# Kernel tuning notes

Measured on AMD Instinct MI355X. Metric: run time of the kernel, lower is better.

Reference implementation:

```python
import jax, jax.numpy as jnp
import numpy as np

B, T, I, H, HORIZON = 64, 512, 256, 1024, 24


def _lstm_layer(x, Wih, Whh, bih, bhh):
    """PyTorch-convention LSTM layer. x: [B,T,I_l] -> outputs [B,T,H].
    Gate order along 4H axis: i, f, g, o."""
    b = x.shape[0]
    h_dim = Whh.shape[1]
    # Precompute input contribution for all timesteps: [B,T,4H]
    xg = jnp.einsum('bti,gi->btg', x, Wih) + bih + bhh

    def step(carry, xg_t):
        h, c = carry
        gates = xg_t + h @ Whh.T  # [B,4H]
        i_g, f_g, g_g, o_g = jnp.split(gates, 4, axis=-1)
        c = jax.nn.sigmoid(f_g) * c + jax.nn.sigmoid(i_g) * jnp.tanh(g_g)
        h = jax.nn.sigmoid(o_g) * jnp.tanh(c)
        return (h, c), h

    h0 = jnp.zeros((b, h_dim), x.dtype)
    (_, _), hs = jax.lax.scan(step, (h0, h0), jnp.swapaxes(xg, 0, 1))
    return jnp.swapaxes(hs, 0, 1)  # [B,T,H]


def setup_inputs() -> dict:
    key = jax.random.key(0)
    ks = jax.random.split(key, 11)
    s_i = 1.0 / np.sqrt(H)  # PyTorch-style uniform-ish scale, use scaled normal
    return {
        'x': jax.random.normal(ks[0], (B, T, I), jnp.float32),
        'W_ih0': jax.random.normal(ks[1], (4 * H, I), jnp.float32) * s_i,
        'W_hh0': jax.random.normal(ks[2], (4 * H, H), jnp.float32) * s_i,
        'b_ih0': jax.random.normal(ks[3], (4 * H,), jnp.float32) * s_i,
        'b_hh0': jax.random.normal(ks[4], (4 * H,), jnp.float32) * s_i,
        'W_ih1': jax.random.normal(ks[5], (4 * H, H), jnp.float32) * s_i,
        'W_hh1': jax.random.normal(ks[6], (4 * H, H), jnp.float32) * s_i,
        'b_ih1': jax.random.normal(ks[7], (4 * H,), jnp.float32) * s_i,
        'b_hh1': jax.random.normal(ks[8], (4 * H,), jnp.float32) * s_i,
        'W_head': jax.random.normal(ks[9], (HORIZON, H), jnp.float32) * s_i,
        'b_head': jax.random.normal(ks[10], (HORIZON,), jnp.float32) * s_i,
    }


def reference(x, W_ih0, W_hh0, b_ih0, b_hh0, W_ih1, W_hh1, b_ih1, b_hh1, W_head, b_head):
    h1 = _lstm_layer(x, W_ih0, W_hh0, b_ih0, b_hh0)   # [B,T,H]
    h2 = _lstm_layer(h1, W_ih1, W_hh1, b_ih1, b_hh1)  # [B,T,H]
    last = h2[:, -1, :]                                # [B,H]
    return last @ W_head.T + b_head                    # [B,HORIZON]
```

## Files before the change

### kernel.cpp

```cpp
#include <hip/hip_runtime.h>


typedef _Float16 h8 __attribute__((ext_vector_type(8)));
typedef float    f4 __attribute__((ext_vector_type(4)));
typedef unsigned long long u64;

#define WS_W0P   0
#define WS_W1P   10485760
#define WS_H0Q   27262976
#define WS_H2Q   27787264
#define WS_SYNC  28049408
#define WS_XPK   28057600
#define WS_XPK_END 44834816ULL

static __device__ __forceinline__ float sigm(float v) { return 1.f / (1.f + __expf(-v)); }
static __device__ __forceinline__ float tanh_fast(float v) {
  const float e = __expf(2.f * v);
  return 1.f - 2.f / (e + 1.f);
}
static __device__ __forceinline__ h8 vload16(const _Float16* p) {
  return *(const volatile h8*)p;
}
static __device__ __forceinline__ void vstore16(_Float16* p, h8 v) {
  *(volatile h8*)p = v;
}

__global__ void prep_kernel(const float* __restrict__ x,
                            const float* __restrict__ Wih0, const float* __restrict__ Whh0,
                            const float* __restrict__ Wih1, const float* __restrict__ Whh1,
                            _Float16* __restrict__ W0p, _Float16* __restrict__ W1p,
                            _Float16* __restrict__ xpk,
                            unsigned* __restrict__ hz, unsigned* __restrict__ sync_ws)
{
  const long tid0 = (long)blockIdx.x * blockDim.x + threadIdx.x;
  const long np   = (long)gridDim.x * blockDim.x;

  for (long e = tid0; e < 5242880; e += np) {
    const int j = e & 7, quad = (e >> 3) & 3, l15 = (e >> 5) & 15, nt = (e >> 9) & 7;
    const int r = (int)(e >> 12);
    const int c = r % 40, cs = r / 40;
    const int col = nt * 16 + l15;
    const int row = (col >> 5) * 1024 + cs * 32 + (col & 31);
    const int k = c * 32 + quad * 8 + j;
    const float v = (k < 256) ? Wih0[(long)row * 256 + k] : Whh0[(long)row * 1024 + k - 256];
    W0p[e] = (_Float16)v;
  }
  for (long e = tid0; e < 8388608; e += np) {
    const int j = e & 7, quad = (e >> 3) & 3, l15 = (e >> 5) & 15, nt = (e >> 9) & 7;
    const int r = (int)(e >> 12);
    const int c = r & 63, cs = r >> 6;
    const int col = nt * 16 + l15;
    const int row = (col >> 5) * 1024 + cs * 32 + (col & 31);
    const int k = c * 32 + quad * 8 + j;
    const float v = (k < 1024) ? Wih1[(long)row * 1024 + k] : Whh1[(long)row * 1024 + k - 1024];
    W1p[e] = (_Float16)v;
  }
  if (xpk) {
    for (long e = tid0; e < 8388608; e += np) {
      const int k32 = e & 31, b16 = (e >> 5) & 15, bg = (e >> 9) & 3;
      const int c = (e >> 11) & 7;
      const int t = (int)(e >> 14);
      const int b = bg * 16 + b16, k = c * 32 + k32;
      xpk[e] = (_Float16)x[(long)b * 131072 + (long)t * 256 + k];
    }
  }
  for (long e = tid0; e < 196608; e += np) hz[e] = 0u;
  if (tid0 < 2048) sync_ws[tid0] = 0u;
}

template<bool XP>
__launch_bounds__(512, 1)
__global__ void lstm_kernel(const float* __restrict__ x, const _Float16* __restrict__ xpk,
                            const float* __restrict__ bih0, const float* __restrict__ bhh0,
                            const float* __restrict__ bih1, const float* __restrict__ bhh1,
                            const _Float16* __restrict__ W0p, const _Float16* __restrict__ W1p,
                            _Float16* __restrict__ h0q, _Float16* __restrict__ h2q,
                            unsigned* __restrict__ sy)
{
  extern __shared__ float gb[];
  __shared__ float cst[512];
  __shared__ float biasl[128];
  __shared__ _Float16 htmp[32 * 18];

  const int tid = threadIdx.x, wg = blockIdx.x;
  const int xcd = wg & 7, jdec = wg >> 3;
  const int lay = jdec & 1, jj = jdec >> 1;
  const int bg = jj & 3, csl = jj >> 2;
  const int cs = xcd * 4 + csl;
  const int lane = tid & 63, kg = tid >> 6;
  const int l15 = lane & 15, quad = lane >> 4;
  const int boff = l15 * 32 + quad * 8;
  const int aoff = bg * 512 + l15 * 32 + quad * 8;

  const _Float16* Wp = lay ? (W1p + (long)cs * 262144) : (W0p + (long)cs * 163840);

  if (tid < 128) {
    const int row = (tid >> 5) * 1024 + cs * 32 + (tid & 31);
    biasl[tid] = lay ? (bih1[row] + bhh1[row]) : (bih0[row] + bhh0[row]);
  }
  cst[tid] = 0.f;
  __syncthreads();

  unsigned* const fL0  = sy + (bg * 32);
  unsigned* const fL1  = sy + ((4 + bg) * 32);
  unsigned* const fOwn = (lay ? fL1 : fL0) + cs;

  auto spin1 = [&](const unsigned* p, int tgt) {
    while ((int)__hip_atomic_load(p, __ATOMIC_RELAXED, __HIP_MEMORY_SCOPE_AGENT) < tgt)
      __builtin_amdgcn_s_sleep(2);
  };

  auto dump = [&](const f4* acc) {
#pragma unroll
    for (int nt = 0; nt < 8; ++nt)
      *(f4*)&gb[(kg * 128 + nt * 16 + l15) * 24 + quad * 4] = acc[nt];
  };

  auto pointwise_publish = [&](_Float16* wr, int n, int gtgt) {
    __syncthreads();
    {
      const int b16 = tid & 15, hh = tid >> 4;
      float gv[4];
#pragma unroll
      for (int gt = 0; gt < 4; ++gt) {
        float s = biasl[gt * 32 + hh];
#pragma unroll
        for (int k = 0; k < 8; ++k) s += gb[(k * 128 + gt * 32 + hh) * 24 + b16];
        gv[gt] = s;
      }
      const float si = sigm(gv[0]), sf = sigm(gv[1]);
      const float tg = tanh_fast(gv[2]), so = sigm(gv[3]);
      const float cn = sf * cst[tid] + si * tg;
      cst[tid] = cn;
      htmp[hh * 18 + b16] = (_Float16)(so * tanh_fast(cn));
    }
    __syncthreads();
    if (tid < 64) {
      if (tid < 32) spin1(fL1 + tid, gtgt);
      const int b16 = tid & 15, q = tid >> 4;
      union { h8 v; _Float16 e[8]; } r;
#pragma unroll
      for (int i = 0; i < 8; ++i) r.e[i] = htmp[(q * 8 + i) * 18 + b16];
      vstore16(wr + (cs * 4 + bg) * 512 + b16 * 32 + q * 8, r.v);
      asm volatile("s_waitcnt vmcnt(0)" ::: "memory");
      if (tid == 0)
        __hip_atomic_store(fOwn, (unsigned)(n + 1),
                           __ATOMIC_RELAXED, __HIP_MEMORY_SCOPE_AGENT);
    }
  };

  if (lay == 0) {
    const int c0 = kg * 5;
    for (int n = 0; n < 512; ++n) {
      const _Float16* h0prev = h0q + ((n - 1) & 3) * 65536;
      const _Float16* xs = XP ? (xpk + (long)n * 16384) : nullptr;

      f4 acc[8] = {};
      h8 Ab[5]; h8 Bb[2][8];
      auto loadB = [&](int c, int sl) {
        const _Float16* bp = Wp + (long)c * 4096 + boff;
#pragma unroll
        for (int nt = 0; nt < 8; ++nt) Bb[sl][nt] = *(const h8*)(bp + nt * 512);
      };
      auto loadA = [&](int c, int idx) {
        if (c < 8) {
          if (XP) Ab[idx] = *(const h8*)(xs + c * 2048 + aoff);
          else {
            const float* q = x + (long)(bg * 16 + l15) * 131072 + (long)n * 256 + c * 32 + quad * 8;
            const f4 v0 = *(const f4*)q;
            const f4 v1 = *(const f4*)(q + 4);
            h8 t;
            t[0]=(_Float16)v0[0]; t[1]=(_Float16)v0[1]; t[2]=(_Float16)v0[2]; t[3]=(_Float16)v0[3];
            t[4]=(_Float16)v1[0]; t[5]=(_Float16)v1[1]; t[6]=(_Float16)v1[2]; t[7]=(_Float16)v1[3];
            Ab[idx] = t;
          }
        } else {
          Ab[idx] = vload16(h0prev + (c - 8) * 2048 + aoff);
        }
      };

      loadB(c0, 0);
#pragma unroll
      for (int i = 0; i < 5; ++i)
        if (c0 + i < 8) loadA(c0 + i, i);

      if (lane < 5) {
        const int c = c0 + lane;
        if (c >= 8) spin1(fL0 + (c - 8), n);
      }

#pragma unroll
      for (int i = 0; i < 5; ++i)
        if (c0 + i >= 8) loadA(c0 + i, i);

#pragma unroll
      for (int i = 0; i < 5; ++i) {
        if (i + 1 < 5) loadB(c0 + i + 1, (i + 1) & 1);
        const h8 A = Ab[i];
#pragma unroll
        for (int nt = 0; nt < 8; ++nt)
          acc[nt] = __builtin_amdgcn_mfma_f32_16x16x32_f16(A, Bb[i & 1][nt], acc[nt], 0, 0, 0);
      }
      dump(acc);
      pointwise_publish(h0q + (n & 3) * 65536, n, n - 3);
    }
  } else {
    const int c0 = kg * 4;
    for (int n = 0; n < 512; ++n) {
      const _Float16* h0cur  = h0q + (n & 3) * 65536;
      const _Float16* h2prev = h2q + ((n - 1) & 1) * 65536;

      f4 acc[8] = {};
      h8 Ab[4]; h8 Bb[2][8];
      auto loadB = [&](int c, int sl) {
        const _Float16* bp = Wp + (long)c * 4096 + boff;
#pragma unroll
        for (int nt = 0; nt < 8; ++nt) Bb[sl][nt] = *(const h8*)(bp + nt * 512);
      };
      auto loadA = [&](const _Float16* hb, int cloc, int idx) {
        Ab[idx] = vload16(hb + cloc * 2048 + aoff);
      };

      loadB(c0, 0);
      if (lane < 4) spin1(fL0 + c0 + lane, n + 1);
#pragma unroll
      for (int i = 0; i < 4; ++i) loadA(h0cur, c0 + i, i);
#pragma unroll
      for (int i = 0; i < 4; ++i) {
        if (i + 1 < 4) loadB(c0 + i + 1, (i + 1) & 1);
        const h8 A = Ab[i];
#pragma unroll
        for (int nt = 0; nt < 8; ++nt)
          acc[nt] = __builtin_amdgcn_mfma_f32_16x16x32_f16(A, Bb[i & 1][nt], acc[nt], 0, 0, 0);
      }

      loadB(32 + c0, 0);
      if (lane < 4) spin1(fL1 + c0 + lane, n);
#pragma unroll
      for (int i = 0; i < 4; ++i) loadA(h2prev, c0 + i, i);
#pragma unroll
      for (int i = 0; i < 4; ++i) {
        if (i + 1 < 4) loadB(32 + c0 + i + 1, (i + 1) & 1);
        const h8 A = Ab[i];
#pragma unroll
        for (int nt = 0; nt < 8; ++nt)
          acc[nt] = __builtin_amdgcn_mfma_f32_16x16x32_f16(A, Bb[i & 1][nt], acc[nt], 0, 0, 0);
      }
      dump(acc);
      pointwise_publish(h2q + (n & 1) * 65536, n, n);
    }
  }
}

__global__ void head_kernel(const _Float16* __restrict__ h2s, const float* __restrict__ Wh,
                            const float* __restrict__ bh, float* __restrict__ out)
{
  const int blk = blockIdx.x;
  const int b = blk / 24, j = blk % 24;
  const int lane = threadIdx.x;
  float sum = 0.f;
#pragma unroll
  for (int k0 = 0; k0 < 1024; k0 += 64) {
    const int hid = k0 + lane;
    const float hv = (float)h2s[((hid >> 5) * 4 + (b >> 4)) * 512 + (b & 15) * 32 + (hid & 31)];
    sum += hv * Wh[(long)j * 1024 + hid];
  }
#pragma unroll
  for (int off = 32; off > 0; off >>= 1)
    sum += __shfl_down(sum, off, 64);
  if (lane == 0) out[b * 24 + j] = sum + bh[j];
}

extern "C" void kernel_launch(void* const* d_in, const int* in_sizes, int n_in,
                              void* d_out, int out_size, void* d_ws, size_t ws_size,
                              hipStream_t stream)
{
  const float* x    = (const float*)d_in[0];
  const float* Wih0 = (const float*)d_in[1];
  const float* Whh0 = (const float*)d_in[2];
  const float* bih0 = (const float*)d_in[3];
  const float* bhh0 = (const float*)d_in[4];
  const float* Wih1 = (const float*)d_in[5];
  const float* Whh1 = (const float*)d_in[6];
  const float* bih1 = (const float*)d_in[7];
  const float* bhh1 = (const float*)d_in[8];
  const float* Whd  = (const float*)d_in[9];
  const float* bhd  = (const float*)d_in[10];

  char* ws = (char*)d_ws;
  _Float16* W0p     = (_Float16*)(ws + WS_W0P);
  _Float16* W1p     = (_Float16*)(ws + WS_W1P);
  _Float16* h0q     = (_Float16*)(ws + WS_H0Q);
  _Float16* h2q     = (_Float16*)(ws + WS_H2Q);
  unsigned* sync_ws = (unsigned*)(ws + WS_SYNC);
  float* out = (float*)d_out;

  const bool use_xpk = (ws_size >= WS_XPK_END);
  _Float16* xpk = use_xpk ? (_Float16*)(ws + WS_XPK) : nullptr;

  prep_kernel<<<dim3(2048), dim3(256), 0, stream>>>(
      x, Wih0, Whh0, Wih1, Whh1, W0p, W1p, xpk,
      (unsigned*)(ws + WS_H0Q), sync_ws);

  if (use_xpk)
    lstm_kernel<true><<<dim3(256), dim3(512), 98304, stream>>>(
        x, xpk, bih0, bhh0, bih1, bhh1, W0p, W1p, h0q, h2q, sync_ws);
  else
    lstm_kernel<false><<<dim3(256), dim3(512), 98304, stream>>>(
        x, nullptr, bih0, bhh0, bih1, bhh1, W0p, W1p, h0q, h2q, sync_ws);

  head_kernel<<<dim3(64 * 24), dim3(64), 0, stream>>>(
      h2q + 65536, Whd, bhd, out);
}
```

Measured before the change: 4.564 ms.

## Free one warp per block from MFMA work and prefetch all B tiles upfront

```diff
diff --git a/kernel.cpp b/kernel.cpp
--- a/kernel.cpp
+++ b/kernel.cpp
@@ -107,13 +107,13 @@
 
   auto spin1 = [&](const unsigned* p, int tgt) {
     while ((int)__hip_atomic_load(p, __ATOMIC_RELAXED, __HIP_MEMORY_SCOPE_AGENT) < tgt)
-      __builtin_amdgcn_s_sleep(2);
+      __builtin_amdgcn_s_sleep(1);
   };
 
   auto dump = [&](const f4* acc) {
 #pragma unroll
     for (int nt = 0; nt < 8; ++nt)
-      *(f4*)&gb[(kg * 128 + nt * 16 + l15) * 24 + quad * 4] = acc[nt];
+      *(f4*)&gb[((kg - 1) * 128 + nt * 16 + l15) * 24 + quad * 4] = acc[nt];
   };
 
   auto pointwise_publish = [&](_Float16* wr, int n, int gtgt) {
@@ -125,7 +125,7 @@
       for (int gt = 0; gt < 4; ++gt) {
         float s = biasl[gt * 32 + hh];
 #pragma unroll
-        for (int k = 0; k < 8; ++k) s += gb[(k * 128 + gt * 32 + hh) * 24 + b16];
+        for (int k = 0; k < 7; ++k) s += gb[(k * 128 + gt * 32 + hh) * 24 + b16];
         gv[gt] = s;
       }
       const float si = sigm(gv[0]), sf = sigm(gv[1]);
@@ -150,103 +150,107 @@
   };
 
   if (lay == 0) {
-    const int c0 = kg * 5;
+    const int c0 = (kg <= 6) ? (kg - 1) * 6 : 35;
+    const int nc = (kg <= 5) ? 6 : 5;
     for (int n = 0; n < 512; ++n) {
-      const _Float16* h0prev = h0q + ((n - 1) & 3) * 65536;
-      const _Float16* xs = XP ? (xpk + (long)n * 16384) : nullptr;
-
-      f4 acc[8] = {};
-      h8 Ab[5]; h8 Bb[2][8];
-      auto loadB = [&](int c, int sl) {
-        const _Float16* bp = Wp + (long)c * 4096 + boff;
-#pragma unroll
-        for (int nt = 0; nt < 8; ++nt) Bb[sl][nt] = *(const h8*)(bp + nt * 512);
-      };
-      auto loadA = [&](int c, int idx) {
-        if (c < 8) {
-          if (XP) Ab[idx] = *(const h8*)(xs + c * 2048 + aoff);
-          else {
-            const float* q = x + (long)(bg * 16 + l15) * 131072 + (long)n * 256 + c * 32 + quad * 8;
-            const f4 v0 = *(const f4*)q;
-            const f4 v1 = *(const f4*)(q + 4);
-            h8 t;
-            t[0]=(_Float16)v0[0]; t[1]=(_Float16)v0[1]; t[2]=(_Float16)v0[2]; t[3]=(_Float16)v0[3];
-            t[4]=(_Float16)v1[0]; t[5]=(_Float16)v1[1]; t[6]=(_Float16)v1[2]; t[7]=(_Float16)v1[3];
-            Ab[idx] = t;
+      if (kg >= 1) {
+        const _Float16* h0prev = h0q + ((n - 1) & 3) * 65536;
+        const _Float16* xs = XP ? (xpk + (long)n * 16384) : nullptr;
+
+        f4 acc[8] = {};
+        h8 Ab[6]; h8 Bb[6][8];
+        auto loadB = [&](int c, int sl) {
+          const _Float16* bp = Wp + (long)c * 4096 + boff;
+#pragma unroll
+          for (int nt = 0; nt < 8; ++nt) Bb[sl][nt] = *(const h8*)(bp + nt * 512);
+        };
+        auto loadA = [&](int c, int idx) {
+          if (c < 8) {
+            if (XP) Ab[idx] = *(const h8*)(xs + c * 2048 + aoff);
+            else {
+              const float* q = x + (long)(bg * 16 + l15) * 131072 + (long)n * 256 + c * 32 + quad * 8;
+              const f4 v0 = *(const f4*)q;
+              const f4 v1 = *(const f4*)(q + 4);
+              h8 t;
+              t[0]=(_Float16)v0[0]; t[1]=(_Float16)v0[1]; t[2]=(_Float16)v0[2]; t[3]=(_Float16)v0[3];
+              t[4]=(_Float16)v1[0]; t[5]=(_Float16)v1[1]; t[6]=(_Float16)v1[2]; t[7]=(_Float16)v1[3];
+              Ab[idx] = t;
+            }
+          } else {
+            Ab[idx] = vload16(h0prev + (c - 8) * 2048 + aoff);
           }
-        } else {
-          Ab[idx] = vload16(h0prev + (c - 8) * 2048 + aoff);
+        };
+
+#pragma unroll
+        for (int i = 0; i < 6; ++i) if (i < nc) loadB(c0 + i, i);
+#pragma unroll
+        for (int i = 0; i < 6; ++i) if (i < nc && (c0 + i) < 8) loadA(c0 + i, i);
+
+        if (lane < nc) {
+          const int c = c0 + lane;
+          if (c >= 8) spin1(fL0 + (c - 8), n);
         }
-      };
-
-      loadB(c0, 0);
-#pragma unroll
-      for (int i = 0; i < 5; ++i)
-        if (c0 + i < 8) loadA(c0 + i, i);
-
-      if (lane < 5) {
-        const int c = c0 + lane;
-        if (c >= 8) spin1(fL0 + (c - 8), n);
+
+#pragma unroll
+        for (int i = 0; i < 6; ++i) if (i < nc && (c0 + i) >= 8) loadA(c0 + i, i);
+
+#pragma unroll
+        for (int i = 0; i < 6; ++i) if (i < nc) {
+          const h8 A = Ab[i];
+#pragma unroll
+          for (int nt = 0; nt < 8; ++nt)
+            acc[nt] = __builtin_amdgcn_mfma_f32_16x16x32_f16(A, Bb[i][nt], acc[nt], 0, 0, 0);
+        }
+        dump(acc);
       }
-
-#pragma unroll
-      for (int i = 0; i < 5; ++i)
-        if (c0 + i >= 8) loadA(c0 + i, i);
-
-#pragma unroll
-      for (int i = 0; i < 5; ++i) {
-        if (i + 1 < 5) loadB(c0 + i + 1, (i + 1) & 1);
-        const h8 A = Ab[i];
-#pragma unroll
-        for (int nt = 0; nt < 8; ++nt)
-          acc[nt] = __builtin_amdgcn_mfma_f32_16x16x32_f16(A, Bb[i & 1][nt], acc[nt], 0, 0, 0);
+      pointwise_publish(h0q + (n & 3) * 65536, n, n - 3);
+    }
+  } else {
+    const int c0 = (kg <= 5) ? (kg - 1) * 5 : 20 + (kg - 5) * 4;
+    const int nc = (kg <= 4) ? 5 : 4;
+    for (int n = 0; n < 512; ++n) {
+      if (kg >= 1) {
+        const _Float16* h0cur  = h0q + (n & 3) * 65536;
+        const _Float16* h2prev = h2q + ((n - 1) & 1) * 65536;
+
+        f4 acc[8] = {};
+        h8 Ab[5]; h8 Bb[5][8];
+        auto loadB = [&](int c, int sl) {
+          const _Float16* bp = Wp + (long)c * 4096 + boff;
+#pragma unroll
+          for (int nt = 0; nt < 8; ++nt) Bb[sl][nt] = *(const h8*)(bp + nt * 512);
+        };
+        auto loadA = [&](const _Float16* hb, int cloc, int idx) {
+          Ab[idx] = vload16(hb + cloc * 2048 + aoff);
+        };
+
+#pragma unroll
+        for (int i = 0; i < 5; ++i) if (i < nc) loadB(c0 + i, i);
+        if (lane < nc) spin1(fL0 + c0 + lane, n + 1);
+#pragma unroll
+        for (int i = 0; i < 5; ++i) if (i < nc) loadA(h0cur, c0 + i, i);
+#pragma unroll
+        for (int i = 0; i < 5; ++i) if (i < nc) {
+          const h8 A = Ab[i];
+#pragma unroll
+          for (int nt = 0; nt < 8; ++nt)
+            acc[nt] = __builtin_amdgcn_mfma_f32_16x16x32_f16(A, Bb[i][nt], acc[nt], 0, 0, 0);
+        }
+
+#pragma unroll
+        for (int i = 0; i < 5; ++i) if (i < nc) loadB(32 + c0 + i, i);
+        if (lane < nc) spin1(fL1 + c0 + lane, n);
+#pragma unroll
+        for (int i = 0; i < 5; ++i) if (i < nc) loadA(h2prev, c0 + i, i);
+#pragma unroll
+        for (int i = 0; i < 5; ++i) if (i < nc) {
+          const h8 A = Ab[i];
+#pragma unroll
+          for (int nt = 0; nt < 8; ++nt)
+            acc[nt] = __builtin_amdgcn_mfma_f32_16x16x32_f16(A, Bb[i][nt], acc[nt], 0, 0, 0);
+        }
+        dump(acc);
       }
-      dump(acc);
-      pointwise_publish(h0q + (n & 3) * 65536, n, n - 3);
-    }
-  } else {
-    const int c0 = kg * 4;
-    for (int n = 0; n < 512; ++n) {
-      const _Float16* h0cur  = h0q + (n & 3) * 65536;
-      const _Float16* h2prev = h2q + ((n - 1) & 1) * 65536;
-
-      f4 acc[8] = {};
-      h8 Ab[4]; h8 Bb[2][8];
-      auto loadB = [&](int c, int sl) {
-        const _Float16* bp = Wp + (long)c * 4096 + boff;
-#pragma unroll
-        for (int nt = 0; nt < 8; ++nt) Bb[sl][nt] = *(const h8*)(bp + nt * 512);
-      };
-      auto loadA = [&](const _Float16* hb, int cloc, int idx) {
-        Ab[idx] = vload16(hb + cloc * 2048 + aoff);
-      };
-
-      loadB(c0, 0);
-      if (lane < 4) spin1(fL0 + c0 + lane, n + 1);
-#pragma unroll
-      for (int i = 0; i < 4; ++i) loadA(h0cur, c0 + i, i);
-#pragma unroll
-      for (int i = 0; i < 4; ++i) {
-        if (i + 1 < 4) loadB(c0 + i + 1, (i + 1) & 1);
-        const h8 A = Ab[i];
-#pragma unroll
-        for (int nt = 0; nt < 8; ++nt)
-          acc[nt] = __builtin_amdgcn_mfma_f32_16x16x32_f16(A, Bb[i & 1][nt], acc[nt], 0, 0, 0);
-      }
-
-      loadB(32 + c0, 0);
-      if (lane < 4) spin1(fL1 + c0 + lane, n);
-#pragma unroll
-      for (int i = 0; i < 4; ++i) loadA(h2prev, c0 + i, i);
-#pragma unroll
-      for (int i = 0; i < 4; ++i) {
-        if (i + 1 < 4) loadB(32 + c0 + i + 1, (i + 1) & 1);
-        const h8 A = Ab[i];
-#pragma unroll
-        for (int nt = 0; nt < 8; ++nt)
-          acc[nt] = __builtin_amdgcn_mfma_f32_16x16x32_f16(A, Bb[i & 1][nt], acc[nt], 0, 0, 0);
-      }
-      dump(acc);
       pointwise_publish(h2q + (n & 1) * 65536, n, n);
     }
   }
@@ -303,10 +307,10 @@
       (unsigned*)(ws + WS_H0Q), sync_ws);
 
   if (use_xpk)
-    lstm_kernel<true><<<dim3(256), dim3(512), 98304, stream>>>(
+    lstm_kernel<true><<<dim3(256), dim3(512), 86016, stream>>>(
         x, xpk, bih0, bhh0, bih1, bhh1, W0p, W1p, h0q, h2q, sync_ws);
   else
-    lstm_kernel<false><<<dim3(256), dim3(512), 98304, stream>>>(
+    lstm_kernel<false><<<dim3(256), dim3(512), 86016, stream>>>(
         x, nullptr, bih0, bhh0, bih1, bhh1, W0p, W1p, h0q, h2q, sync_ws);
 
   head_kernel<<<dim3(64 * 24), dim3(64), 0, stream>>>(
```

New measurement: 10.89 ms. 139% more time.
